# Kernel tuning notes

Hardware: AMD Instinct MI355X
Metric: run time of the kernel (lower is better)

Reference implementation:

```python
import jax, jax.numpy as jnp
import numpy as np

# Hardcoded 6-node part graph from the module (src, dst) pairs; PyG flows src->dst.
_EDGES = np.array([[0,1],[0,2],[0,3],[0,4],[0,5],[1,2],[1,3],[1,4],[1,5],[2,3],[2,4],[3,5],[4,5],[1,0],[2,0],[3,0],[4,0],[5,0],[2,1],[3,1],[4,1],[5,1],[3,2],[4,2],[5,3],[5,4]], dtype=np.int32)
SRC = jnp.asarray(_EDGES[:, 0])
DST = jnp.asarray(_EDGES[:, 1])
NUM_NODES = 6


def setup_inputs() -> dict:
    key = jax.random.key(0)
    k0, k1, k2 = jax.random.split(key, 3)
    C, B = 128, 32768
    x = jax.random.normal(k0, (NUM_NODES, B, C), dtype=jnp.float32)
    # SAGEConv weights: lin_l (aggregated neighbors, carries bias) and lin_r (root)
    W_l = jax.random.normal(k1, (2 * C, C), dtype=jnp.float32) / np.sqrt(C).astype(np.float32)
    W_r = jax.random.normal(k2, (2 * C, C), dtype=jnp.float32) / np.sqrt(C).astype(np.float32)
    b = jnp.zeros((2 * C,), dtype=jnp.float32)
    return {"x": x, "W_l": W_l, "W_r": W_r, "b": b}


def reference(x, W_l, W_r, b):
    # x: [N=6, B, C]
    # mean aggregation of source features at each destination node
    msg = x[SRC]                                                  # [E, B, C]
    agg = jax.ops.segment_sum(msg, DST, num_segments=NUM_NODES)   # [N, B, C]
    deg = jax.ops.segment_sum(jnp.ones_like(DST, dtype=x.dtype), DST, num_segments=NUM_NODES)
    agg = agg / deg[:, None, None]
    # SAGEConv: lin_l(agg) + lin_r(x), bias in lin_l
    y = jnp.einsum('nbc,oc->nbo', agg, W_l) + b + jnp.einsum('nbc,oc->nbo', x, W_r)
    y = jax.nn.gelu(y, approximate=False)                         # torch F.gelu = exact erf
    # Python cat-loop over nodes == concatenate the 6 node slices along features
    N, B, O = y.shape
    return jnp.transpose(y, (1, 0, 2)).reshape(B, N * O)          # [B, 6*2C]
```

## Files before the change

kernel.cpp:

```cpp
#include <hip/hip_runtime.h>
#include <hip/hip_bf16.h>

#define NB 32768
#define CD 128
#define NNODES 6
#define OUTW 1536
#define KW 256

typedef __attribute__((ext_vector_type(8))) short short8;
typedef __attribute__((ext_vector_type(4))) float f32x4;

static __device__ __forceinline__ short f2bf(float f) {
    union { __bf16 b; short s; } u;
    u.b = (__bf16)f;
    return u.s;
}

static __device__ __forceinline__ short8 pack8(f32x4 a, f32x4 b) {
    short8 p;
    #pragma unroll
    for (int j = 0; j < 4; ++j) { p[j] = f2bf(a[j]); p[4 + j] = f2bf(b[j]); }
    return p;
}

__global__ void prep_w(const float* __restrict__ Wl, const float* __restrict__ Wr,
                       short* __restrict__ Wb) {
    const int i = (blockIdx.x * 256 + threadIdx.x) * 8;
    const int o = i >> 8;
    const int k = i & 255;
    const float* src = (k < 128) ? (Wl + o * CD + k) : (Wr + o * CD + (k - 128));
    *(short8*)(Wb + i) = pack8(*(const f32x4*)src, *(const f32x4*)(src + 4));
}

#define LIDX(p, r, k) ((((p) << 11) + ((r) << 7) + (k)) ^ (((r) & 7) << 3))

__global__ __launch_bounds__(256, 2)
void sage_v5(const float* __restrict__ x, const short* __restrict__ Wb,
             const float* __restrict__ bias, float* __restrict__ out) {
    __shared__ __align__(16) short A[10 * 16 * 128];

    const int t = threadIdx.x;
    const size_t row0 = (size_t)blockIdx.x * 16;

    {
        const int r = t >> 4;
        const int c = t & 15;
        const float* pb = x + (row0 + r) * CD + c * 8;
        f32x4 a0 = *(const f32x4*)(pb + 0ull * (NB * CD)), c0 = *(const f32x4*)(pb + 0ull * (NB * CD) + 4);
        f32x4 a1 = *(const f32x4*)(pb + 1ull * (NB * CD)), c1 = *(const f32x4*)(pb + 1ull * (NB * CD) + 4);
        f32x4 a2 = *(const f32x4*)(pb + 2ull * (NB * CD)), c2 = *(const f32x4*)(pb + 2ull * (NB * CD) + 4);
        f32x4 a3 = *(const f32x4*)(pb + 3ull * (NB * CD)), c3 = *(const f32x4*)(pb + 3ull * (NB * CD) + 4);
        f32x4 a4 = *(const f32x4*)(pb + 4ull * (NB * CD)), c4 = *(const f32x4*)(pb + 4ull * (NB * CD) + 4);
        f32x4 a5 = *(const f32x4*)(pb + 5ull * (NB * CD)), c5 = *(const f32x4*)(pb + 5ull * (NB * CD) + 4);

        f32x4 S01a = a0 + a1, S01c = c0 + c1;
        f32x4 S25a = a2 + a5, S25c = c2 + c5;
        f32x4 S34a = a3 + a4, S34c = c3 + c4;
        f32x4 Ta = S01a + S25a + S34a, Tc = S01c + S25c + S34c;

        const int k = c * 8;
        *(short8*)&A[LIDX(0, r, k)] = pack8((Ta - a0) * 0.2f,  (Tc - c0) * 0.2f);
        *(short8*)&A[LIDX(1, r, k)] = pack8((Ta - a1) * 0.2f,  (Tc - c1) * 0.2f);
        *(short8*)&A[LIDX(2, r, k)] = pack8((S01a + S34a) * 0.25f, (S01c + S34c) * 0.25f);
        *(short8*)&A[LIDX(3, r, k)] = pack8((S01a + S25a) * 0.25f, (S01c + S25c) * 0.25f);
        *(short8*)&A[LIDX(4, r, k)] = pack8(a0, c0);
        *(short8*)&A[LIDX(5, r, k)] = pack8(a1, c1);
        *(short8*)&A[LIDX(6, r, k)] = pack8(a2, c2);
        *(short8*)&A[LIDX(7, r, k)] = pack8(a3, c3);
        *(short8*)&A[LIDX(8, r, k)] = pack8(a4, c4);
        *(short8*)&A[LIDX(9, r, k)] = pack8(a5, c5);
    }
    __syncthreads();

    const int lane = t & 63;
    const int wv = t >> 6;
    const int lo = lane & 15;
    const int hi = lane >> 4;
    const int obase = wv * 64;

    f32x4 acc[NNODES][4];
    #pragma unroll
    for (int n = 0; n < NNODES; ++n)
        #pragma unroll
        for (int i = 0; i < 4; ++i) acc[n][i] = (f32x4){0.f, 0.f, 0.f, 0.f};

    #pragma unroll
    for (int m = 0; m < 4; ++m) {
        const int kk = m * 32 + hi * 8;
        short8 fg0 = *(const short8*)&A[LIDX(0, lo, kk)];
        short8 fg1 = *(const short8*)&A[LIDX(1, lo, kk)];
        short8 fg25 = *(const short8*)&A[LIDX(2, lo, kk)];
        short8 fg34 = *(const short8*)&A[LIDX(3, lo, kk)];
        short8 fx[NNODES];
        #pragma unroll
        for (int s = 0; s < NNODES; ++s)
            fx[s] = *(const short8*)&A[LIDX(4 + s, lo, kk)];

        #pragma unroll
        for (int i = 0; i < 4; ++i) {
            const int o = obase + i * 16 + lo;
            short8 wa = *(const short8*)&Wb[o * KW + kk];
            short8 wx = *(const short8*)&Wb[o * KW + 128 + kk];
            acc[0][i] = __builtin_amdgcn_mfma_f32_16x16x32_bf16(wa, fg0,  acc[0][i], 0, 0, 0);
            acc[1][i] = __builtin_amdgcn_mfma_f32_16x16x32_bf16(wa, fg1,  acc[1][i], 0, 0, 0);
            acc[2][i] = __builtin_amdgcn_mfma_f32_16x16x32_bf16(wa, fg25, acc[2][i], 0, 0, 0);
            acc[3][i] = __builtin_amdgcn_mfma_f32_16x16x32_bf16(wa, fg34, acc[3][i], 0, 0, 0);
            acc[4][i] = __builtin_amdgcn_mfma_f32_16x16x32_bf16(wa, fg34, acc[4][i], 0, 0, 0);
            acc[5][i] = __builtin_amdgcn_mfma_f32_16x16x32_bf16(wa, fg25, acc[5][i], 0, 0, 0);
            #pragma unroll
            for (int n = 0; n < NNODES; ++n)
                acc[n][i] = __builtin_amdgcn_mfma_f32_16x16x32_bf16(wx, fx[n], acc[n][i], 0, 0, 0);
        }
    }

    #pragma unroll
    for (int n = 0; n < NNODES; ++n) {
        #pragma unroll
        for (int i = 0; i < 4; ++i) {
            f32x4 bv = *(const f32x4*)&bias[obase + i * 16 + hi * 4];
            f32x4 v = acc[n][i] + bv;
            f32x4 g;
            #pragma unroll
            for (int j = 0; j < 4; ++j) {
                const float s = v[j] * (0.7978845608f + 0.0356774081f * v[j] * v[j]);
                const float r = __builtin_amdgcn_exp2f(-2.885390082f * s);
                g[j] = v[j] * __builtin_amdgcn_rcpf(1.0f + r);
            }
            *(f32x4*)&out[(row0 + lo) * OUTW + n * 256 + obase + i * 16 + hi * 4] = g;
        }
    }
}

extern "C" void kernel_launch(void* const* d_in, const int* in_sizes, int n_in,
                              void* d_out, int out_size, void* d_ws, size_t ws_size,
                              hipStream_t stream) {
    const float* x  = (const float*)d_in[0];
    const float* Wl = (const float*)d_in[1];
    const float* Wr = (const float*)d_in[2];
    const float* b  = (const float*)d_in[3];
    float* out = (float*)d_out;
    short* Wb = (short*)d_ws;

    prep_w<<<dim3(32), dim3(256), 0, stream>>>(Wl, Wr, Wb);
    sage_v5<<<dim3(NB / 16), dim3(256), 0, stream>>>(x, Wb, b, out);
}
```

Before: 96.75 us.

## Split node outputs across two wave groups with 512-thread blocks and nontemporal stores

```diff
diff --git a/kernel.cpp b/kernel.cpp
--- a/kernel.cpp
+++ b/kernel.cpp
@@ -8,6 +8,7 @@
 #define KW 256
 
 typedef __attribute__((ext_vector_type(8))) short short8;
+typedef __attribute__((ext_vector_type(4))) short s16x4;
 typedef __attribute__((ext_vector_type(4))) float f32x4;
 
 static __device__ __forceinline__ short f2bf(float f) {
@@ -23,6 +24,13 @@
     return p;
 }
 
+static __device__ __forceinline__ s16x4 pack4(f32x4 a) {
+    s16x4 p;
+    #pragma unroll
+    for (int j = 0; j < 4; ++j) p[j] = f2bf(a[j]);
+    return p;
+}
+
 __global__ void prep_w(const float* __restrict__ Wl, const float* __restrict__ Wr,
                        short* __restrict__ Wb) {
     const int i = (blockIdx.x * 256 + threadIdx.x) * 8;
@@ -34,8 +42,8 @@
 
 #define LIDX(p, r, k) ((((p) << 11) + ((r) << 7) + (k)) ^ (((r) & 7) << 3))
 
-__global__ __launch_bounds__(256, 2)
-void sage_v5(const float* __restrict__ x, const short* __restrict__ Wb,
+__global__ __launch_bounds__(512, 4)
+void sage_v6(const float* __restrict__ x, const short* __restrict__ Wb,
              const float* __restrict__ bias, float* __restrict__ out) {
     __shared__ __align__(16) short A[10 * 16 * 128];
 
@@ -43,82 +51,78 @@
     const size_t row0 = (size_t)blockIdx.x * 16;
 
     {
-        const int r = t >> 4;
-        const int c = t & 15;
-        const float* pb = x + (row0 + r) * CD + c * 8;
-        f32x4 a0 = *(const f32x4*)(pb + 0ull * (NB * CD)), c0 = *(const f32x4*)(pb + 0ull * (NB * CD) + 4);
-        f32x4 a1 = *(const f32x4*)(pb + 1ull * (NB * CD)), c1 = *(const f32x4*)(pb + 1ull * (NB * CD) + 4);
-        f32x4 a2 = *(const f32x4*)(pb + 2ull * (NB * CD)), c2 = *(const f32x4*)(pb + 2ull * (NB * CD) + 4);
-        f32x4 a3 = *(const f32x4*)(pb + 3ull * (NB * CD)), c3 = *(const f32x4*)(pb + 3ull * (NB * CD) + 4);
-        f32x4 a4 = *(const f32x4*)(pb + 4ull * (NB * CD)), c4 = *(const f32x4*)(pb + 4ull * (NB * CD) + 4);
-        f32x4 a5 = *(const f32x4*)(pb + 5ull * (NB * CD)), c5 = *(const f32x4*)(pb + 5ull * (NB * CD) + 4);
-
-        f32x4 S01a = a0 + a1, S01c = c0 + c1;
-        f32x4 S25a = a2 + a5, S25c = c2 + c5;
-        f32x4 S34a = a3 + a4, S34c = c3 + c4;
-        f32x4 Ta = S01a + S25a + S34a, Tc = S01c + S25c + S34c;
-
-        const int k = c * 8;
-        *(short8*)&A[LIDX(0, r, k)] = pack8((Ta - a0) * 0.2f,  (Tc - c0) * 0.2f);
-        *(short8*)&A[LIDX(1, r, k)] = pack8((Ta - a1) * 0.2f,  (Tc - c1) * 0.2f);
-        *(short8*)&A[LIDX(2, r, k)] = pack8((S01a + S34a) * 0.25f, (S01c + S34c) * 0.25f);
-        *(short8*)&A[LIDX(3, r, k)] = pack8((S01a + S25a) * 0.25f, (S01c + S25c) * 0.25f);
-        *(short8*)&A[LIDX(4, r, k)] = pack8(a0, c0);
-        *(short8*)&A[LIDX(5, r, k)] = pack8(a1, c1);
-        *(short8*)&A[LIDX(6, r, k)] = pack8(a2, c2);
-        *(short8*)&A[LIDX(7, r, k)] = pack8(a3, c3);
-        *(short8*)&A[LIDX(8, r, k)] = pack8(a4, c4);
-        *(short8*)&A[LIDX(9, r, k)] = pack8(a5, c5);
+        const int r = t >> 5;
+        const int c = t & 31;
+        const float* pb = x + (row0 + r) * CD + c * 4;
+        f32x4 v0 = *(const f32x4*)(pb + 0ull * (NB * CD));
+        f32x4 v1 = *(const f32x4*)(pb + 1ull * (NB * CD));
+        f32x4 v2 = *(const f32x4*)(pb + 2ull * (NB * CD));
+        f32x4 v3 = *(const f32x4*)(pb + 3ull * (NB * CD));
+        f32x4 v4 = *(const f32x4*)(pb + 4ull * (NB * CD));
+        f32x4 v5 = *(const f32x4*)(pb + 5ull * (NB * CD));
+        f32x4 S01 = v0 + v1, S25 = v2 + v5, S34 = v3 + v4;
+        f32x4 T = S01 + S25 + S34;
+        const int k = c * 4;
+        *(s16x4*)&A[LIDX(0, r, k)] = pack4((T - v0) * 0.2f);
+        *(s16x4*)&A[LIDX(1, r, k)] = pack4((T - v1) * 0.2f);
+        *(s16x4*)&A[LIDX(2, r, k)] = pack4((S01 + S34) * 0.25f);
+        *(s16x4*)&A[LIDX(3, r, k)] = pack4((S01 + S25) * 0.25f);
+        *(s16x4*)&A[LIDX(4, r, k)] = pack4(v0);
+        *(s16x4*)&A[LIDX(5, r, k)] = pack4(v1);
+        *(s16x4*)&A[LIDX(6, r, k)] = pack4(v2);
+        *(s16x4*)&A[LIDX(7, r, k)] = pack4(v3);
+        *(s16x4*)&A[LIDX(8, r, k)] = pack4(v4);
+        *(s16x4*)&A[LIDX(9, r, k)] = pack4(v5);
     }
     __syncthreads();
 
     const int lane = t & 63;
     const int wv = t >> 6;
+    const int ng = wv >> 2;
+    const int strip = wv & 3;
     const int lo = lane & 15;
     const int hi = lane >> 4;
-    const int obase = wv * 64;
+    const int paA = ng ? 3 : 0;
+    const int paB = ng ? 3 : 1;
+    const int pxb = 4 + ng * 3;
 
-    f32x4 acc[NNODES][4];
+    f32x4 acc[3][4];
     #pragma unroll
-    for (int n = 0; n < NNODES; ++n)
+    for (int n = 0; n < 3; ++n)
         #pragma unroll
         for (int i = 0; i < 4; ++i) acc[n][i] = (f32x4){0.f, 0.f, 0.f, 0.f};
 
     #pragma unroll
     for (int m = 0; m < 4; ++m) {
         const int kk = m * 32 + hi * 8;
-        short8 fg0 = *(const short8*)&A[LIDX(0, lo, kk)];
-        short8 fg1 = *(const short8*)&A[LIDX(1, lo, kk)];
-        short8 fg25 = *(const short8*)&A[LIDX(2, lo, kk)];
-        short8 fg34 = *(const short8*)&A[LIDX(3, lo, kk)];
-        short8 fx[NNODES];
-        #pragma unroll
-        for (int s = 0; s < NNODES; ++s)
-            fx[s] = *(const short8*)&A[LIDX(4 + s, lo, kk)];
+        short8 fgA = *(const short8*)&A[LIDX(paA, lo, kk)];
+        short8 fgB = *(const short8*)&A[LIDX(paB, lo, kk)];
+        short8 fgC = *(const short8*)&A[LIDX(2,   lo, kk)];
+        short8 fx0 = *(const short8*)&A[LIDX(pxb + 0, lo, kk)];
+        short8 fx1 = *(const short8*)&A[LIDX(pxb + 1, lo, kk)];
+        short8 fx2 = *(const short8*)&A[LIDX(pxb + 2, lo, kk)];
 
         #pragma unroll
         for (int i = 0; i < 4; ++i) {
-            const int o = obase + i * 16 + lo;
+            const int o = strip * 64 + i * 16 + lo;
             short8 wa = *(const short8*)&Wb[o * KW + kk];
             short8 wx = *(const short8*)&Wb[o * KW + 128 + kk];
-            acc[0][i] = __builtin_amdgcn_mfma_f32_16x16x32_bf16(wa, fg0,  acc[0][i], 0, 0, 0);
-            acc[1][i] = __builtin_amdgcn_mfma_f32_16x16x32_bf16(wa, fg1,  acc[1][i], 0, 0, 0);
-            acc[2][i] = __builtin_amdgcn_mfma_f32_16x16x32_bf16(wa, fg25, acc[2][i], 0, 0, 0);
-            acc[3][i] = __builtin_amdgcn_mfma_f32_16x16x32_bf16(wa, fg34, acc[3][i], 0, 0, 0);
-            acc[4][i] = __builtin_amdgcn_mfma_f32_16x16x32_bf16(wa, fg34, acc[4][i], 0, 0, 0);
-            acc[5][i] = __builtin_amdgcn_mfma_f32_16x16x32_bf16(wa, fg25, acc[5][i], 0, 0, 0);
-            #pragma unroll
-            for (int n = 0; n < NNODES; ++n)
-                acc[n][i] = __builtin_amdgcn_mfma_f32_16x16x32_bf16(wx, fx[n], acc[n][i], 0, 0, 0);
+            acc[0][i] = __builtin_amdgcn_mfma_f32_16x16x32_bf16(wa, fgA, acc[0][i], 0, 0, 0);
+            acc[1][i] = __builtin_amdgcn_mfma_f32_16x16x32_bf16(wa, fgB, acc[1][i], 0, 0, 0);
+            acc[2][i] = __builtin_amdgcn_mfma_f32_16x16x32_bf16(wa, fgC, acc[2][i], 0, 0, 0);
+            acc[0][i] = __builtin_amdgcn_mfma_f32_16x16x32_bf16(wx, fx0, acc[0][i], 0, 0, 0);
+            acc[1][i] = __builtin_amdgcn_mfma_f32_16x16x32_bf16(wx, fx1, acc[1][i], 0, 0, 0);
+            acc[2][i] = __builtin_amdgcn_mfma_f32_16x16x32_bf16(wx, fx2, acc[2][i], 0, 0, 0);
         }
     }
 
     #pragma unroll
-    for (int n = 0; n < NNODES; ++n) {
+    for (int n = 0; n < 3; ++n) {
         #pragma unroll
         for (int i = 0; i < 4; ++i) {
-            f32x4 bv = *(const f32x4*)&bias[obase + i * 16 + hi * 4];
-            f32x4 v = acc[n][i] + bv;
+            const int ocol = strip * 64 + i * 16 + hi * 4;
+            const int col = (ng * 3 + n) * 256 + ocol;
+            f32x4 v = acc[n][i] + *(const f32x4*)&bias[ocol];
             f32x4 g;
             #pragma unroll
             for (int j = 0; j < 4; ++j) {
@@ -126,7 +130,7 @@
                 const float r = __builtin_amdgcn_exp2f(-2.885390082f * s);
                 g[j] = v[j] * __builtin_amdgcn_rcpf(1.0f + r);
             }
-            *(f32x4*)&out[(row0 + lo) * OUTW + n * 256 + obase + i * 16 + hi * 4] = g;
+            __builtin_nontemporal_store(g, (f32x4*)&out[(row0 + lo) * OUTW + col]);
         }
     }
 }
@@ -142,5 +146,5 @@
     short* Wb = (short*)d_ws;
 
     prep_w<<<dim3(32), dim3(256), 0, stream>>>(Wl, Wr, Wb);
-    sage_v5<<<dim3(NB / 16), dim3(256), 0, stream>>>(x, Wb, b, out);
+    sage_v6<<<dim3(NB / 16), dim3(512), 0, stream>>>(x, Wb, b, out);
 }
```

Measured after the change: 117.3 us. +21.3%, slower.
